# Optimization experiments

Measured on AMD Instinct MI355X. Metric: run time of the kernel, lower is better.

## Reference

```python
import jax, jax.numpy as jnp
import numpy as np

TEMPERATURE = 8.0  # sqrt(head_dim=64)

def setup_inputs() -> dict:
    key = jax.random.key(0)
    kq, kk, kv, km, kb = jax.random.split(key, 5)
    B, H, S, D = 2, 16, 2048, 64
    q = jax.random.normal(kq, (B, H, S, D), dtype=jnp.float32)
    k = jax.random.normal(kk, (B, H, S, D), dtype=jnp.float32)
    v = jax.random.normal(kv, (B, H, S, D), dtype=jnp.float32)
    mask = jax.random.randint(km, (B, 1, S, S), 0, 2).astype(bool)
    attn_bias = jax.random.normal(kb, (1, H, S, S), dtype=jnp.float32)
    return {"q": q, "k": k, "v": v, "mask": mask, "attn_bias": attn_bias}

def reference(q, k, v, mask, attn_bias):
    # scores: [B,H,Sq,Sk]
    attn = jnp.einsum("bhqd,bhkd->bhqk", q, k) / TEMPERATURE
    attn = attn + attn_bias
    attn = jnp.where(mask, -jnp.inf, attn)  # masked_fill(mask, -inf)
    attn = jax.nn.softmax(attn, axis=-1)
    # dropout in eval mode (deterministic) -> identity
    out = jnp.einsum("bhqk,bhkd->bhqd", attn, v)
    return (out, attn)
```

## Files before the change

### kernel.cpp

```cpp
#include <hip/hip_runtime.h>

#define BATCH 2
#define NH    16
#define SEQ   2048
#define DH    64
#define NW    8
#define KSPAN 256
#define CHUNK 64
#define NCHK  (KSPAN/CHUNK)
#define SUBT  32

typedef __attribute__((ext_vector_type(8))) short          bf16x8;
typedef __attribute__((ext_vector_type(4))) float          f32x4;
typedef __attribute__((ext_vector_type(2))) unsigned int   u32x2;
typedef __attribute__((ext_vector_type(4))) int            i32x4;

__device__ __forceinline__ unsigned short f2bf(float f) {
    union { float f; unsigned int i; } c;
    c.f = f;
    unsigned int x = c.i;
    x += 0x7fffu + ((x >> 16) & 1u);
    return (unsigned short)(x >> 16);
}
__device__ __forceinline__ unsigned int pkt(float lo, float hi) {
    union { float f; unsigned int u; } a, b;
    a.f = lo; b.f = hi;
    return (b.u & 0xFFFF0000u) | (a.u >> 16);
}
__device__ __forceinline__ float bfu2f(unsigned short u) {
    union { unsigned int i; float f; } c;
    c.i = ((unsigned int)u) << 16;
    return c.f;
}

template<bool ISBYTE>
__global__ __launch_bounds__(512, 2)
void sdpa_fused(const float* __restrict__ qp,
                const float* __restrict__ kp,
                const float* __restrict__ vp,
                const void*  __restrict__ mp,
                const float* __restrict__ bp,
                float* __restrict__ outp,
                float* __restrict__ attnp)
{
    __shared__ __align__(16) unsigned short Pbig[16 * 2048];
    __shared__ __align__(16) float Arena[NW][16 * CHUNK];
    __shared__ float Lsum[NW][16];

    const int tid  = threadIdx.x;
    const int w    = tid >> 6;
    const int lane = tid & 63;
    const int l15  = lane & 15;
    const int g    = lane >> 4;

    const unsigned int* mw = (const unsigned int*)mp;
    if ((__any((int)(mw[lane & 31] > 1u)) != 0) != ISBYTE) return;

    const int bid  = blockIdx.x;
    const int orig = (bid & 7) * 512 + (bid >> 3);
    const int h    = orig >> 8;
    const int rem  = orig & 255;
    const int qt   = rem >> 1;
    const int b    = rem & 1;
    const int bh   = b * NH + h;
    const int qbase = qt * 16;
    const int kw   = w * KSPAN;

    const float* kbh = kp + (size_t)bh * SEQ * DH;
    const float* vbh = vp + (size_t)bh * SEQ * DH;
    char* pivot = (char*)&Arena[w][0];
    char* pbig  = (char*)Pbig;

    bf16x8 qf0, qf1;
    {
        const float* qb = qp + ((size_t)bh * SEQ + qbase + l15) * DH + g * 8;
        #pragma unroll
        for (int j = 0; j < 8; ++j) {
            qf0[j] = (short)f2bf(qb[j]      * 0.125f);
            qf1[j] = (short)f2bf(qb[32 + j] * 0.125f);
        }
    }

    struct KS { f32x4 k[2][4]; };
    auto load_k = [&](int tk, KS& R) {
        const int kb = kw + tk * SUBT;
        #pragma unroll
        for (int mb = 0; mb < 2; ++mb) {
            const float* arow = kbh + (size_t)(kb + 16 * mb + l15) * DH + g * 8;
            R.k[mb][0] = *(const f32x4*)(arow);
            R.k[mb][1] = *(const f32x4*)(arow + 4);
            R.k[mb][2] = *(const f32x4*)(arow + 32);
            R.k[mb][3] = *(const f32x4*)(arow + 36);
        }
    };

    auto produce = [&](const KS& R, int s2) {
        #pragma unroll
        for (int mb = 0; mb < 2; ++mb) {
            union { bf16x8 v; unsigned int u[4]; } A0, A1;
            A0.u[0] = pkt(R.k[mb][0][0], R.k[mb][0][1]);
            A0.u[1] = pkt(R.k[mb][0][2], R.k[mb][0][3]);
            A0.u[2] = pkt(R.k[mb][1][0], R.k[mb][1][1]);
            A0.u[3] = pkt(R.k[mb][1][2], R.k[mb][1][3]);
            A1.u[0] = pkt(R.k[mb][2][0], R.k[mb][2][1]);
            A1.u[1] = pkt(R.k[mb][2][2], R.k[mb][2][3]);
            A1.u[2] = pkt(R.k[mb][3][0], R.k[mb][3][1]);
            A1.u[3] = pkt(R.k[mb][3][2], R.k[mb][3][3]);
            f32x4 c = (f32x4){0.f, 0.f, 0.f, 0.f};
            __builtin_amdgcn_s_setprio(1);
            c = __builtin_amdgcn_mfma_f32_16x16x32_bf16(A0.v, qf0, c, 0, 0, 0);
            c = __builtin_amdgcn_mfma_f32_16x16x32_bf16(A1.v, qf1, c, 0, 0, 0);
            __builtin_amdgcn_s_setprio(0);
            const int byo = (128 * s2 + 64 * mb + 16 * g) ^ ((l15 & 7) << 4);
            *(f32x4*)(pivot + l15 * 256 + byo) = c;
        }
    };

    auto load_bias = [&](int c, f32x4* B) {
        #pragma unroll
        for (int i = 0; i < 4; ++i)
            B[i] = *(const f32x4*)(bp + ((size_t)h * SEQ + qbase + 4 * i + g) * SEQ
                                   + kw + c * CHUNK + 4 * l15);
    };

    float rs[4] = {0.f, 0.f, 0.f, 0.f};

    auto consume = [&](int c, const f32x4* B) {
        #pragma unroll
        for (int i = 0; i < 4; ++i) {
            const int qr = 4 * i + g;
            int m4[4];
            if constexpr (ISBYTE) {
                unsigned int mk = *(const unsigned int*)((const unsigned char*)mp +
                    ((size_t)b * SEQ + qbase + qr) * SEQ + kw + c * CHUNK + 4 * l15);
                #pragma unroll
                for (int j = 0; j < 4; ++j) m4[j] = (int)((mk >> (8 * j)) & 0xFFu);
            } else {
                i32x4 mk = *(const i32x4*)((const int*)mp +
                    ((size_t)b * SEQ + qbase + qr) * SEQ + kw + c * CHUNK + 4 * l15);
                #pragma unroll
                for (int j = 0; j < 4; ++j) m4[j] = mk[j];
            }
            f32x4 p = *(const f32x4*)(pivot + qr * 256 + ((16 * l15) ^ ((qr & 7) << 4)));
            f32x4 pa;
            #pragma unroll
            for (int j = 0; j < 4; ++j)
                pa[j] = m4[j] ? 0.0f : __expf(p[j] + B[i][j]);
            rs[i] += pa[0] + pa[1] + pa[2] + pa[3];
            u32x2 pw;
            pw[0] = pkt(pa[0], pa[1]);
            pw[1] = pkt(pa[2], pa[3]);
            const int byo = (2 * kw + 128 * c + 8 * l15) ^ ((qr & 7) << 4);
            *(u32x2*)(pbig + qr * 4096 + byo) = pw;
        }
    };

    f32x4 accO[4];
    #pragma unroll
    for (int i = 0; i < 4; ++i) accO[i] = (f32x4){0.f, 0.f, 0.f, 0.f};

    auto pv = [&](int c) {
        #pragma unroll
        for (int ks2 = 0; ks2 < 2; ++ks2) {
            const int colg = kw + (2 * c + ks2) * SUBT;
            const int byo = (2 * colg + 16 * g) ^ ((l15 & 7) << 4);
            bf16x8 pf = *(const bf16x8*)(pbig + l15 * 4096 + byo);
            const float* vb2 = vbh + (size_t)colg * DH + 512 * g + l15;
            union { bf16x8 v; unsigned int u[4]; } vf[4];
            #pragma unroll
            for (int nb = 0; nb < 4; ++nb)
                #pragma unroll
                for (int i2 = 0; i2 < 4; ++i2)
                    vf[nb].u[i2] = pkt(vb2[(2 * i2) * 64 + 16 * nb],
                                       vb2[(2 * i2 + 1) * 64 + 16 * nb]);
            __builtin_amdgcn_s_setprio(1);
            #pragma unroll
            for (int nb = 0; nb < 4; ++nb)
                accO[nb] = __builtin_amdgcn_mfma_f32_16x16x32_bf16(pf, vf[nb].v, accO[nb], 0, 0, 0);
            __builtin_amdgcn_s_setprio(0);
        }
    };

    {
        KS RA, RB;
        f32x4 BA[4], BB[4];
        load_k(0, RA);
        load_k(1, RB);
        load_bias(0, BA);

        #pragma unroll
        for (int c = 0; c < NCHK; ++c) {
            f32x4* Bcur = (c & 1) ? BB : BA;
            f32x4* Bnxt = (c & 1) ? BA : BB;
            if (c < NCHK - 1) load_bias(c + 1, Bnxt);
            produce(RA, 0);  load_k((2 * c + 2) & 7, RA);
            produce(RB, 1);  load_k((2 * c + 3) & 7, RB);
            consume(c, Bcur);
            pv(c);
        }
    }

    #pragma unroll
    for (int i = 0; i < 4; ++i) {
        float t = rs[i];
        t += __shfl_xor(t, 1, 64);
        t += __shfl_xor(t, 2, 64);
        t += __shfl_xor(t, 4, 64);
        t += __shfl_xor(t, 8, 64);
        if (l15 == 0) Lsum[w][4 * i + g] = t;
    }
    #pragma unroll
    for (int rr = 0; rr < 4; ++rr)
        #pragma unroll
        for (int nb = 0; nb < 4; ++nb)
            Arena[w][(4 * g + rr) * 64 + 16 * nb + l15] = accO[nb][rr];

    __syncthreads();

    float rv[4];
    #pragma unroll
    for (int i = 0; i < 4; ++i) {
        float s = 0.f;
        #pragma unroll
        for (int ww = 0; ww < NW; ++ww) s += Lsum[ww][4 * i + g];
        rv[i] = 1.0f / s;
    }

    #pragma unroll
    for (int i = 0; i < 4; ++i) {
        const int qr = 4 * i + g;
        #pragma unroll
        for (int u = 0; u < 2; ++u) {
            const int byo = (2 * kw + 256 * u + 16 * l15) ^ ((qr & 7) << 4);
            bf16x8 pb8 = *(const bf16x8*)(pbig + qr * 4096 + byo);
            f32x4 o0, o1;
            #pragma unroll
            for (int j = 0; j < 4; ++j) {
                o0[j] = bfu2f((unsigned short)pb8[j])     * rv[i];
                o1[j] = bfu2f((unsigned short)pb8[4 + j]) * rv[i];
            }
            float* ap = attnp + ((size_t)bh * SEQ + qbase + qr) * SEQ
                        + kw + u * 128 + 8 * l15;
            *(f32x4*)ap       = o0;
            *(f32x4*)(ap + 4) = o1;
        }
    }

    if (w == 0) {
        const int d = lane;
        #pragma unroll
        for (int r = 0; r < 16; ++r) {
            float s = 0.f, o = 0.f;
            #pragma unroll
            for (int ww = 0; ww < NW; ++ww) {
                s += Lsum[ww][r];
                o += Arena[ww][r * 64 + d];
            }
            outp[((size_t)bh * SEQ + qbase + r) * DH + d] = o / s;
        }
    }
}

extern "C" void kernel_launch(void* const* d_in, const int* in_sizes, int n_in,
                              void* d_out, int out_size, void* d_ws, size_t ws_size,
                              hipStream_t stream) {
    const float* qp = (const float*)d_in[0];
    const float* kp = (const float*)d_in[1];
    const float* vp = (const float*)d_in[2];
    const void*  mp = d_in[3];
    const float* bp = (const float*)d_in[4];

    float* outp  = (float*)d_out;
    float* attnp = outp + (size_t)BATCH * NH * SEQ * DH;

    dim3 grid(BATCH * NH * (SEQ / 16)), block(512);
    sdpa_fused<true ><<<grid, block, 0, stream>>>(qp, kp, vp, mp, bp, outp, attnp);
    sdpa_fused<false><<<grid, block, 0, stream>>>(qp, kp, vp, mp, bp, outp, attnp);
}
```

Baseline: 551.3 us.

## Halve query rows per block to 8 and raise occupancy to four blocks per CU

Each block now handles 8 query rows instead of 16, with shared memory buffers shrunk to match, twice as many blocks in the grid, and launch bounds raised to 4 blocks per CU. The MFMA tiles stay 16 wide, so half of each QK^T and PV MFMA computes duplicated rows that are then discarded. K and V are loaded and converted twice as often per query row. The trade is more wasted MFMA work and redundant K/V traffic in exchange for higher occupancy and lower LDS use per block.

Result: slower. 1.537 ms (+178.9%).

```diff
diff --git a/kernel.cpp b/kernel.cpp
--- a/kernel.cpp
+++ b/kernel.cpp
@@ -5,6 +5,7 @@
 #define SEQ   2048
 #define DH    64
 #define NW    8
+#define QR    8
 #define KSPAN 256
 #define CHUNK 64
 #define NCHK  (KSPAN/CHUNK)
@@ -34,7 +35,7 @@
 }
 
 template<bool ISBYTE>
-__global__ __launch_bounds__(512, 2)
+__global__ __launch_bounds__(512, 4)
 void sdpa_fused(const float* __restrict__ qp,
                 const float* __restrict__ kp,
                 const float* __restrict__ vp,
@@ -43,9 +44,9 @@
                 float* __restrict__ outp,
                 float* __restrict__ attnp)
 {
-    __shared__ __align__(16) unsigned short Pbig[16 * 2048];
-    __shared__ __align__(16) float Arena[NW][16 * CHUNK];
-    __shared__ float Lsum[NW][16];
+    __shared__ __align__(16) unsigned short Pbig[QR * 2048];
+    __shared__ __align__(16) float Arena[NW][QR * 64];
+    __shared__ float Lsum[NW][QR];
 
     const int tid  = threadIdx.x;
     const int w    = tid >> 6;
@@ -57,13 +58,13 @@
     if ((__any((int)(mw[lane & 31] > 1u)) != 0) != ISBYTE) return;
 
     const int bid  = blockIdx.x;
-    const int orig = (bid & 7) * 512 + (bid >> 3);
-    const int h    = orig >> 8;
-    const int rem  = orig & 255;
+    const int orig = (bid & 7) * 1024 + (bid >> 3);
+    const int h    = orig >> 9;
+    const int rem  = orig & 511;
     const int qt   = rem >> 1;
     const int b    = rem & 1;
     const int bh   = b * NH + h;
-    const int qbase = qt * 16;
+    const int qbase = qt * QR;
     const int kw   = w * KSPAN;
 
     const float* kbh = kp + (size_t)bh * SEQ * DH;
@@ -73,7 +74,7 @@
 
     bf16x8 qf0, qf1;
     {
-        const float* qb = qp + ((size_t)bh * SEQ + qbase + l15) * DH + g * 8;
+        const float* qb = qp + ((size_t)bh * SEQ + qbase + (l15 & 7)) * DH + g * 8;
         #pragma unroll
         for (int j = 0; j < 8; ++j) {
             qf0[j] = (short)f2bf(qb[j]      * 0.125f);
@@ -111,23 +112,25 @@
             c = __builtin_amdgcn_mfma_f32_16x16x32_bf16(A0.v, qf0, c, 0, 0, 0);
             c = __builtin_amdgcn_mfma_f32_16x16x32_bf16(A1.v, qf1, c, 0, 0, 0);
             __builtin_amdgcn_s_setprio(0);
-            const int byo = (128 * s2 + 64 * mb + 16 * g) ^ ((l15 & 7) << 4);
-            *(f32x4*)(pivot + l15 * 256 + byo) = c;
+            if (l15 < 8) {
+                const int byo = (128 * s2 + 64 * mb + 16 * g) ^ (l15 << 4);
+                *(f32x4*)(pivot + l15 * 256 + byo) = c;
+            }
         }
     };
 
     auto load_bias = [&](int c, f32x4* B) {
         #pragma unroll
-        for (int i = 0; i < 4; ++i)
+        for (int i = 0; i < 2; ++i)
             B[i] = *(const f32x4*)(bp + ((size_t)h * SEQ + qbase + 4 * i + g) * SEQ
                                    + kw + c * CHUNK + 4 * l15);
     };
 
-    float rs[4] = {0.f, 0.f, 0.f, 0.f};
+    float rs[2] = {0.f, 0.f};
 
     auto consume = [&](int c, const f32x4* B) {
         #pragma unroll
-        for (int i = 0; i < 4; ++i) {
+        for (int i = 0; i < 2; ++i) {
             const int qr = 4 * i + g;
             int m4[4];
             if constexpr (ISBYTE) {
@@ -141,7 +144,7 @@
                 #pragma unroll
                 for (int j = 0; j < 4; ++j) m4[j] = mk[j];
             }
-            f32x4 p = *(const f32x4*)(pivot + qr * 256 + ((16 * l15) ^ ((qr & 7) << 4)));
+            f32x4 p = *(const f32x4*)(pivot + qr * 256 + ((16 * l15) ^ (qr << 4)));
             f32x4 pa;
             #pragma unroll
             for (int j = 0; j < 4; ++j)
@@ -150,7 +153,7 @@
             u32x2 pw;
             pw[0] = pkt(pa[0], pa[1]);
             pw[1] = pkt(pa[2], pa[3]);
-            const int byo = (2 * kw + 128 * c + 8 * l15) ^ ((qr & 7) << 4);
+            const int byo = (2 * kw + 128 * c + 8 * l15) ^ (qr << 4);
             *(u32x2*)(pbig + qr * 4096 + byo) = pw;
         }
     };
@@ -164,7 +167,7 @@
         for (int ks2 = 0; ks2 < 2; ++ks2) {
             const int colg = kw + (2 * c + ks2) * SUBT;
             const int byo = (2 * colg + 16 * g) ^ ((l15 & 7) << 4);
-            bf16x8 pf = *(const bf16x8*)(pbig + l15 * 4096 + byo);
+            bf16x8 pf = *(const bf16x8*)(pbig + (l15 & 7) * 4096 + byo);
             const float* vb2 = vbh + (size_t)colg * DH + 512 * g + l15;
             union { bf16x8 v; unsigned int u[4]; } vf[4];
             #pragma unroll
@@ -183,7 +186,7 @@
 
     {
         KS RA, RB;
-        f32x4 BA[4], BB[4];
+        f32x4 BA[2], BB[2];
         load_k(0, RA);
         load_k(1, RB);
         load_bias(0, BA);
@@ -201,7 +204,7 @@
     }
 
     #pragma unroll
-    for (int i = 0; i < 4; ++i) {
+    for (int i = 0; i < 2; ++i) {
         float t = rs[i];
         t += __shfl_xor(t, 1, 64);
         t += __shfl_xor(t, 2, 64);
@@ -209,17 +212,19 @@
         t += __shfl_xor(t, 8, 64);
         if (l15 == 0) Lsum[w][4 * i + g] = t;
     }
-    #pragma unroll
-    for (int rr = 0; rr < 4; ++rr)
-        #pragma unroll
-        for (int nb = 0; nb < 4; ++nb)
-            Arena[w][(4 * g + rr) * 64 + 16 * nb + l15] = accO[nb][rr];
+    if (g < 2) {
+        #pragma unroll
+        for (int rr = 0; rr < 4; ++rr)
+            #pragma unroll
+            for (int nb = 0; nb < 4; ++nb)
+                Arena[w][(4 * g + rr) * 64 + 16 * nb + l15] = accO[nb][rr];
+    }
 
     __syncthreads();
 
-    float rv[4];
-    #pragma unroll
-    for (int i = 0; i < 4; ++i) {
+    float rv[2];
+    #pragma unroll
+    for (int i = 0; i < 2; ++i) {
         float s = 0.f;
         #pragma unroll
         for (int ww = 0; ww < NW; ++ww) s += Lsum[ww][4 * i + g];
@@ -227,11 +232,11 @@
     }
 
     #pragma unroll
-    for (int i = 0; i < 4; ++i) {
+    for (int i = 0; i < 2; ++i) {
         const int qr = 4 * i + g;
         #pragma unroll
         for (int u = 0; u < 2; ++u) {
-            const int byo = (2 * kw + 256 * u + 16 * l15) ^ ((qr & 7) << 4);
+            const int byo = (2 * kw + 256 * u + 16 * l15) ^ (qr << 4);
             bf16x8 pb8 = *(const bf16x8*)(pbig + qr * 4096 + byo);
             f32x4 o0, o1;
             #pragma unroll
@@ -249,7 +254,7 @@
     if (w == 0) {
         const int d = lane;
         #pragma unroll
-        for (int r = 0; r < 16; ++r) {
+        for (int r = 0; r < QR; ++r) {
             float s = 0.f, o = 0.f;
             #pragma unroll
             for (int ww = 0; ww < NW; ++ww) {
@@ -273,7 +278,7 @@
     float* outp  = (float*)d_out;
     float* attnp = outp + (size_t)BATCH * NH * SEQ * DH;
 
-    dim3 grid(BATCH * NH * (SEQ / 16)), block(512);
+    dim3 grid(BATCH * NH * (SEQ / QR)), block(512);
     sdpa_fused<true ><<<grid, block, 0, stream>>>(qp, kp, vp, mp, bp, outp, attnp);
     sdpa_fused<false><<<grid, block, 0, stream>>>(qp, kp, vp, mp, bp, outp, attnp);
 }
```

## Stage V tiles through LDS transpose with coalesced prefetched global loads

Applied to the files above, without the earlier changes.

Replaces the per-lane scattered scalar global loads of V (strided across rows) with coalesced 16-byte loads, prefetched one subtile ahead in registers. Each subtile is converted to bf16 by truncation and written transposed into a per-wave LDS buffer with padded stride, then read back as bf16x8 MFMA operands. This targets uncoalesced global traffic and packing ALU work in the PV step. In exchange it adds LDS usage (about 40 KB), more registers for the prefetch buffer, and truncation instead of round-to-nearest for V. It also relies on implicit intra-wave ordering between LDS writes and reads without an explicit barrier, and it issues one redundant V load after the last subtile.

Measured after the change: 705.2 us. +27.9%, slower.

```diff
diff --git a/kernel.cpp b/kernel.cpp
--- a/kernel.cpp
+++ b/kernel.cpp
@@ -9,6 +9,7 @@
 #define CHUNK 64
 #define NCHK  (KSPAN/CHUNK)
 #define SUBT  32
+#define VSTR  40
 
 typedef __attribute__((ext_vector_type(8))) short          bf16x8;
 typedef __attribute__((ext_vector_type(4))) float          f32x4;
@@ -26,6 +27,11 @@
     union { float f; unsigned int u; } a, b;
     a.f = lo; b.f = hi;
     return (b.u & 0xFFFF0000u) | (a.u >> 16);
+}
+__device__ __forceinline__ unsigned short f2bft(float f) {
+    union { float f; unsigned int u; } c;
+    c.f = f;
+    return (unsigned short)(c.u >> 16);
 }
 __device__ __forceinline__ float bfu2f(unsigned short u) {
     union { unsigned int i; float f; } c;
@@ -45,6 +51,7 @@
 {
     __shared__ __align__(16) unsigned short Pbig[16 * 2048];
     __shared__ __align__(16) float Arena[NW][16 * CHUNK];
+    __shared__ __align__(16) unsigned short VTs[NW][DH * VSTR];
     __shared__ float Lsum[NW][16];
 
     const int tid  = threadIdx.x;
@@ -70,6 +77,7 @@
     const float* vbh = vp + (size_t)bh * SEQ * DH;
     char* pivot = (char*)&Arena[w][0];
     char* pbig  = (char*)Pbig;
+    unsigned short* vt = &VTs[w][0];
 
     bf16x8 qf0, qf1;
     {
@@ -155,38 +163,44 @@
         }
     };
 
+    auto gload_v = [&](int colg, f32x4* Gv) {
+        const float* src = vbh + (size_t)colg * DH;
+        #pragma unroll
+        for (int q = 0; q < 8; ++q)
+            Gv[q] = *(const f32x4*)(src + q * 256 + lane * 4);
+    };
+    auto stage_v = [&](const f32x4* Gv) {
+        #pragma unroll
+        for (int q = 0; q < 8; ++q)
+            #pragma unroll
+            for (int jj = 0; jj < 4; ++jj)
+                vt[(4 * (lane & 15) + jj) * VSTR + 4 * q + (lane >> 4)] = f2bft(Gv[q][jj]);
+    };
+
     f32x4 accO[4];
     #pragma unroll
     for (int i = 0; i < 4; ++i) accO[i] = (f32x4){0.f, 0.f, 0.f, 0.f};
 
-    auto pv = [&](int c) {
-        #pragma unroll
-        for (int ks2 = 0; ks2 < 2; ++ks2) {
-            const int colg = kw + (2 * c + ks2) * SUBT;
-            const int byo = (2 * colg + 16 * g) ^ ((l15 & 7) << 4);
-            bf16x8 pf = *(const bf16x8*)(pbig + l15 * 4096 + byo);
-            const float* vb2 = vbh + (size_t)colg * DH + 512 * g + l15;
-            union { bf16x8 v; unsigned int u[4]; } vf[4];
-            #pragma unroll
-            for (int nb = 0; nb < 4; ++nb)
-                #pragma unroll
-                for (int i2 = 0; i2 < 4; ++i2)
-                    vf[nb].u[i2] = pkt(vb2[(2 * i2) * 64 + 16 * nb],
-                                       vb2[(2 * i2 + 1) * 64 + 16 * nb]);
-            __builtin_amdgcn_s_setprio(1);
-            #pragma unroll
-            for (int nb = 0; nb < 4; ++nb)
-                accO[nb] = __builtin_amdgcn_mfma_f32_16x16x32_bf16(pf, vf[nb].v, accO[nb], 0, 0, 0);
-            __builtin_amdgcn_s_setprio(0);
-        }
+    auto pv_sub = [&](int colg) {
+        const int byo = (2 * colg + 16 * g) ^ ((l15 & 7) << 4);
+        bf16x8 pf = *(const bf16x8*)(pbig + l15 * 4096 + byo);
+        __builtin_amdgcn_s_setprio(1);
+        #pragma unroll
+        for (int nb = 0; nb < 4; ++nb) {
+            bf16x8 vf = *(const bf16x8*)(&vt[(16 * nb + l15) * VSTR + 8 * g]);
+            accO[nb] = __builtin_amdgcn_mfma_f32_16x16x32_bf16(pf, vf, accO[nb], 0, 0, 0);
+        }
+        __builtin_amdgcn_s_setprio(0);
     };
 
     {
         KS RA, RB;
         f32x4 BA[4], BB[4];
+        f32x4 Gv[8];
         load_k(0, RA);
         load_k(1, RB);
         load_bias(0, BA);
+        gload_v(kw, Gv);
 
         #pragma unroll
         for (int c = 0; c < NCHK; ++c) {
@@ -196,7 +210,12 @@
             produce(RA, 0);  load_k((2 * c + 2) & 7, RA);
             produce(RB, 1);  load_k((2 * c + 3) & 7, RB);
             consume(c, Bcur);
-            pv(c);
+            stage_v(Gv);
+            gload_v(kw + (2 * c + 1) * SUBT, Gv);
+            pv_sub(kw + (2 * c) * SUBT);
+            stage_v(Gv);
+            gload_v(kw + (((2 * c + 2) & 7) * SUBT), Gv);
+            pv_sub(kw + (2 * c + 1) * SUBT);
         }
     }
 
```

## Store QK scores as fp16 in LDS and reuse P buffer for output reduction

Applied to the files above, without the earlier changes.

Per-wave score scratch now holds the QK^T tile as fp16 instead of fp32, halving that arena. The row sums reuse the same arena after the main loop, and the cross-wave output reduction reuses the Pbig buffer once attn has been written, separated by extra barriers. This shrinks per-block LDS to about 80KB, likely so two 512-thread blocks fit per CU as the launch bounds request. The cost is lower score precision before exp and two extra block-wide syncs in the epilogue.

Result: slower. 605.2 us (+9.8%).

```diff
diff --git a/kernel.cpp b/kernel.cpp
--- a/kernel.cpp
+++ b/kernel.cpp
@@ -14,6 +14,7 @@
 typedef __attribute__((ext_vector_type(4))) float          f32x4;
 typedef __attribute__((ext_vector_type(2))) unsigned int   u32x2;
 typedef __attribute__((ext_vector_type(4))) int            i32x4;
+typedef __attribute__((ext_vector_type(4))) _Float16       f16x4;
 
 __device__ __forceinline__ unsigned short f2bf(float f) {
     union { float f; unsigned int i; } c;
@@ -44,8 +45,7 @@
                 float* __restrict__ attnp)
 {
     __shared__ __align__(16) unsigned short Pbig[16 * 2048];
-    __shared__ __align__(16) float Arena[NW][16 * CHUNK];
-    __shared__ float Lsum[NW][16];
+    __shared__ __align__(16) unsigned short ArenaH[NW][16 * 64];
 
     const int tid  = threadIdx.x;
     const int w    = tid >> 6;
@@ -68,7 +68,7 @@
 
     const float* kbh = kp + (size_t)bh * SEQ * DH;
     const float* vbh = vp + (size_t)bh * SEQ * DH;
-    char* pivot = (char*)&Arena[w][0];
+    char* pivot = (char*)&ArenaH[w][0];
     char* pbig  = (char*)Pbig;
 
     bf16x8 qf0, qf1;
@@ -111,8 +111,11 @@
             c = __builtin_amdgcn_mfma_f32_16x16x32_bf16(A0.v, qf0, c, 0, 0, 0);
             c = __builtin_amdgcn_mfma_f32_16x16x32_bf16(A1.v, qf1, c, 0, 0, 0);
             __builtin_amdgcn_s_setprio(0);
-            const int byo = (128 * s2 + 64 * mb + 16 * g) ^ ((l15 & 7) << 4);
-            *(f32x4*)(pivot + l15 * 256 + byo) = c;
+            union { f16x4 h; u32x2 u; } hc;
+            hc.h[0] = (_Float16)c[0];  hc.h[1] = (_Float16)c[1];
+            hc.h[2] = (_Float16)c[2];  hc.h[3] = (_Float16)c[3];
+            const int byo = (64 * s2 + 32 * mb + 8 * g) ^ ((l15 & 7) << 4);
+            *(u32x2*)(pivot + l15 * 128 + byo) = hc.u;
         }
     };
 
@@ -141,11 +144,12 @@
                 #pragma unroll
                 for (int j = 0; j < 4; ++j) m4[j] = mk[j];
             }
-            f32x4 p = *(const f32x4*)(pivot + qr * 256 + ((16 * l15) ^ ((qr & 7) << 4)));
+            union { u32x2 u; f16x4 hh; } hv;
+            hv.u = *(const u32x2*)(pivot + qr * 128 + ((8 * l15) ^ ((qr & 7) << 4)));
             f32x4 pa;
             #pragma unroll
             for (int j = 0; j < 4; ++j)
-                pa[j] = m4[j] ? 0.0f : __expf(p[j] + B[i][j]);
+                pa[j] = m4[j] ? 0.0f : __expf((float)hv.hh[j] + B[i][j]);
             rs[i] += pa[0] + pa[1] + pa[2] + pa[3];
             u32x2 pw;
             pw[0] = pkt(pa[0], pa[1]);
@@ -200,20 +204,18 @@
         }
     }
 
-    #pragma unroll
-    for (int i = 0; i < 4; ++i) {
-        float t = rs[i];
-        t += __shfl_xor(t, 1, 64);
-        t += __shfl_xor(t, 2, 64);
-        t += __shfl_xor(t, 4, 64);
-        t += __shfl_xor(t, 8, 64);
-        if (l15 == 0) Lsum[w][4 * i + g] = t;
-    }
-    #pragma unroll
-    for (int rr = 0; rr < 4; ++rr)
-        #pragma unroll
-        for (int nb = 0; nb < 4; ++nb)
-            Arena[w][(4 * g + rr) * 64 + 16 * nb + l15] = accO[nb][rr];
+    {
+        float* lsw = (float*)&ArenaH[w][0];
+        #pragma unroll
+        for (int i = 0; i < 4; ++i) {
+            float t = rs[i];
+            t += __shfl_xor(t, 1, 64);
+            t += __shfl_xor(t, 2, 64);
+            t += __shfl_xor(t, 4, 64);
+            t += __shfl_xor(t, 8, 64);
+            if (l15 == 0) lsw[4 * i + g] = t;
+        }
+    }
 
     __syncthreads();
 
@@ -222,7 +224,7 @@
     for (int i = 0; i < 4; ++i) {
         float s = 0.f;
         #pragma unroll
-        for (int ww = 0; ww < NW; ++ww) s += Lsum[ww][4 * i + g];
+        for (int ww = 0; ww < NW; ++ww) s += ((const float*)&ArenaH[ww][0])[4 * i + g];
         rv[i] = 1.0f / s;
     }
 
@@ -246,6 +248,19 @@
         }
     }
 
+    __syncthreads();
+
+    {
+        float* dep = (float*)pbig + w * 1024;
+        #pragma unroll
+        for (int rr = 0; rr < 4; ++rr)
+            #pragma unroll
+            for (int nb = 0; nb < 4; ++nb)
+                dep[(4 * g + rr) * 64 + 16 * nb + l15] = accO[nb][rr];
+    }
+
+    __syncthreads();
+
     if (w == 0) {
         const int d = lane;
         #pragma unroll
@@ -253,8 +268,8 @@
             float s = 0.f, o = 0.f;
             #pragma unroll
             for (int ww = 0; ww < NW; ++ww) {
-                s += Lsum[ww][r];
-                o += Arena[ww][r * 64 + d];
+                s += ((const float*)&ArenaH[ww][0])[r];
+                o += ((const float*)pbig)[ww * 1024 + r * 64 + d];
             }
             outp[((size_t)bh * SEQ + qbase + r) * DH + d] = o / s;
         }
```
